# Kernel tuning notes

Measured on AMD Instinct MI355X. Metric: run time of the kernel, lower is better.

Reference implementation:

```python
import jax, jax.numpy as jnp
import numpy as np
import math

M = 0.5
S = 64.0
COS_M = math.cos(M)
SIN_M = math.sin(M)
THRESHOLD = math.cos(math.pi - M)
MM = math.sin(math.pi - M) * M

B, D, N_CLASSES = 512, 512, 100000


def setup_inputs() -> dict:
    key = jax.random.key(0)
    k1, k2, k3 = jax.random.split(key, 3)
    embeddings = jax.random.normal(k1, (B, D), dtype=jnp.float32)
    labels = jax.random.randint(k2, (B,), 0, N_CLASSES, dtype=jnp.int32)
    kernel = jax.random.normal(k3, (D, N_CLASSES), dtype=jnp.float32) * 0.05
    t = jnp.zeros((), dtype=jnp.float32)
    return {"embeddings": embeddings, "labels": labels, "kernel": kernel, "t": t}


def reference(embeddings, labels, kernel, t):
    # L2 normalize embeddings (rows) and kernel (columns)
    emb = embeddings / jnp.linalg.norm(embeddings, axis=1, keepdims=True)
    kn = kernel / jnp.linalg.norm(kernel, axis=0, keepdims=True)
    cos_theta = jnp.clip(emb @ kn, -1.0, 1.0)  # [B, C]

    b = cos_theta.shape[0]
    rows = jnp.arange(b)
    target_logit = cos_theta[rows, labels][:, None]  # [B, 1]
    sin_theta = jnp.sqrt(1.0 - jnp.square(target_logit))
    cos_theta_m = target_logit * COS_M - sin_theta * SIN_M  # [B, 1]

    mask = cos_theta > cos_theta_m  # [B, C] hard examples
    final_target_logit = jnp.where(target_logit > THRESHOLD,
                                   cos_theta_m, target_logit - MM)  # [B, 1]

    # EMA update of t (assigned before the hard-example scaling in TF code)
    new_t = 0.01 * jnp.mean(target_logit) + 0.99 * t

    # hard examples: c -> c * (t + c); others unchanged
    cos_theta = jnp.where(mask, cos_theta * (new_t + cos_theta), cos_theta)
    # overwrite label column with the margin-adjusted target logit
    cos_theta = cos_theta.at[rows, labels].set(final_target_logit[:, 0])
    return cos_theta * S
```

## Files before the change

kernel.cpp:

```cpp
#include <hip/hip_runtime.h>
#include <hip/hip_bf16.h>
#include <cstdint>
#include <cstddef>

#define C_N 100000
#define B_N 512
#define D_N 512

#define COS_M_F   0.87758256189037276f
#define SIN_M_F   0.47942553860420301f
#define THRESH_F  (-0.87758256189037276f)
#define MM_F      0.23971276930210150f
#define S_F       64.0f

typedef __attribute__((ext_vector_type(8))) short short8;
typedef __attribute__((ext_vector_type(4))) float f32x4;

__device__ __forceinline__ unsigned short f2bf(float f) {
  unsigned u = __float_as_uint(f);
  u = u + 0x7fffu + ((u >> 16) & 1u);
  return (unsigned short)(u >> 16);
}

__device__ __forceinline__ float wave_sum(float v) {
#pragma unroll
  for (int o = 32; o > 0; o >>= 1) v += __shfl_down(v, o, 64);
  return v;
}

__device__ __forceinline__ void lds_load16(const void* g, void* l) {
  __builtin_amdgcn_global_load_lds(
      (const __attribute__((address_space(1))) unsigned int*)g,
      (__attribute__((address_space(3))) unsigned int*)l, 16, 0, 0);
}

__global__ void embnorm_k(const float* __restrict__ emb, unsigned short* __restrict__ embn,
                          float* __restrict__ rinv) {
  int row = blockIdx.x;
  int t = threadIdx.x;
  float4 v = ((const float4*)(emb + (size_t)row * D_N))[t];
  float ss = v.x * v.x + v.y * v.y + v.z * v.z + v.w * v.w;
  ss = wave_sum(ss);
  __shared__ float red[2];
  if ((t & 63) == 0) red[t >> 6] = ss;
  __syncthreads();
  float tot = red[0] + red[1];
  float ri = rsqrtf(tot);
  if (t == 0) rinv[row] = ri;
  ushort4 o;
  o.x = f2bf(v.x * ri); o.y = f2bf(v.y * ri); o.z = f2bf(v.z * ri); o.w = f2bf(v.w * ri);
  ((ushort4*)(embn + (size_t)row * D_N))[t] = o;
}

__global__ void target2_k(const float* __restrict__ emb, const float* __restrict__ Kp,
                          const float* __restrict__ rinv, const int* __restrict__ labels,
                          float* __restrict__ target, float* __restrict__ ctm,
                          float* __restrict__ ft) {
  int row = blockIdx.x;
  int t = threadIdx.x;
  int lab = labels[row];
  float p = 0.f, ss = 0.f;
  for (int d = t; d < D_N; d += 256) {
    float kv = Kp[(size_t)d * C_N + lab];
    p = fmaf(emb[(size_t)row * D_N + d], kv, p);
    ss = fmaf(kv, kv, ss);
  }
  p = wave_sum(p);
  ss = wave_sum(ss);
  __shared__ float redp[4], reds[4];
  if ((t & 63) == 0) { redp[t >> 6] = p; reds[t >> 6] = ss; }
  __syncthreads();
  if (t == 0) {
    float dot = redp[0] + redp[1] + redp[2] + redp[3];
    float sums = reds[0] + reds[1] + reds[2] + reds[3];
    float tg = dot * rinv[row] * rsqrtf(fmaxf(sums, 1e-30f));
    tg = fminf(fmaxf(tg, -1.f), 1.f);
    float st = sqrtf(fmaxf(1.f - tg * tg, 0.f));
    float cm = tg * COS_M_F - st * SIN_M_F;
    float f = (tg > THRESH_F) ? cm : (tg - MM_F);
    target[row] = tg;
    ctm[row] = cm;
    ft[row] = f;
  }
}

__global__ void newt_k(const float* __restrict__ target, const float* __restrict__ t_in,
                       float* __restrict__ newt) {
  int t = threadIdx.x;
  float v = target[t];
  v = wave_sum(v);
  __shared__ float red[8];
  if ((t & 63) == 0) red[t >> 6] = v;
  __syncthreads();
  if (t == 0) {
    float s = 0.f;
#pragma unroll
    for (int i = 0; i < 8; ++i) s += red[i];
    *newt = 0.01f * (s / (float)B_N) + 0.99f * t_in[0];
  }
}

__launch_bounds__(512, 2)
__global__ void gemm3_k(const float* __restrict__ Kp,
                        const unsigned short* __restrict__ embn,
                        const int* __restrict__ labels,
                        const float* __restrict__ ctm, const float* __restrict__ ft,
                        const float* __restrict__ newt_p, float* __restrict__ out) {
  __shared__ __align__(16) char lds[131072 + 3 * 2048 + 256];
  unsigned short* Bl = (unsigned short*)lds;
  unsigned short* Albase = (unsigned short*)(lds + 65536);
  float* ssum = (float*)(lds + 65536);
  int*   slab = (int*)(lds + 131072);
  float* sctm = (float*)(lds + 131072 + 2048);
  float* sft  = (float*)(lds + 131072 + 4096);
  float* cns  = (float*)(lds + 131072 + 6144);

  const int t = threadIdx.x;
  const int j0 = blockIdx.x * 64;

  slab[t] = labels[t];
  sctm[t] = ctm[t];
  sft[t]  = ft[t];

  const int jq = t & 15;
  const int dr = t >> 4;
  const int jcol = min((j0 >> 2) + jq, (C_N >> 2) - 1);
  const float4* __restrict__ Kv = (const float4*)Kp;
  float4 v[16];
#pragma unroll
  for (int i = 0; i < 16; ++i)
    v[i] = Kv[(size_t)(dr * 16 + i) * (C_N / 4) + jcol];

  float s0 = 0.f, s1 = 0.f, s2 = 0.f, s3 = 0.f;
#pragma unroll
  for (int i = 0; i < 16; ++i) {
    s0 = fmaf(v[i].x, v[i].x, s0);
    s1 = fmaf(v[i].y, v[i].y, s1);
    s2 = fmaf(v[i].z, v[i].z, s2);
    s3 = fmaf(v[i].w, v[i].w, s3);
  }
  ssum[dr * 64 + jq * 4 + 0] = s0;
  ssum[dr * 64 + jq * 4 + 1] = s1;
  ssum[dr * 64 + jq * 4 + 2] = s2;
  ssum[dr * 64 + jq * 4 + 3] = s3;
  __syncthreads();
  if (t < 64) {
    float s = 0.f;
#pragma unroll
    for (int d = 0; d < 32; ++d) s += ssum[d * 64 + t];
    cns[t] = rsqrtf(fmaxf(s, 1e-30f));
  }
  __syncthreads();

  const int l = t & 63, w = t >> 6;
  const int sidx = (l & 7) ^ (l >> 3);
  const int r0 = ((l >> 3) << 1) | (sidx >> 2);
  const int kc8 = (sidx & 3) * 8;
  const unsigned short* asrc = embn + (size_t)(w * 64 + r0) * D_N + kc8;

#pragma unroll
  for (int p = 0; p < 4; ++p)
    lds_load16(asrc + p * 16 * D_N, Albase + w * 2048 + p * 512);

  {
    const float rc0 = cns[jq * 4 + 0];
    const float rc1 = cns[jq * 4 + 1];
    const float rc2 = cns[jq * 4 + 2];
    const float rc3 = cns[jq * 4 + 3];
    const int itile = dr >> 1;
    const int cbase = (dr & 1) * 2;
#pragma unroll
    for (int cc = 0; cc < 4; ++cc) {
      const int n = jq * 4 + cc;
      const int rowp = n >> 1;
      const int nb = (n & 1) << 2;
      const int x7 = rowp & 7;
      const float rc = (cc == 0) ? rc0 : (cc == 1) ? rc1 : (cc == 2) ? rc2 : rc3;
#pragma unroll
      for (int h = 0; h < 2; ++h) {
        unsigned w0 = (unsigned)f2bf(v[h * 8 + 0][cc] * rc) | ((unsigned)f2bf(v[h * 8 + 1][cc] * rc) << 16);
        unsigned w1 = (unsigned)f2bf(v[h * 8 + 2][cc] * rc) | ((unsigned)f2bf(v[h * 8 + 3][cc] * rc) << 16);
        unsigned w2 = (unsigned)f2bf(v[h * 8 + 4][cc] * rc) | ((unsigned)f2bf(v[h * 8 + 5][cc] * rc) << 16);
        unsigned w3 = (unsigned)f2bf(v[h * 8 + 6][cc] * rc) | ((unsigned)f2bf(v[h * 8 + 7][cc] * rc) << 16);
        char* dst = (char*)Bl + itile * 4096 + rowp * 128 + ((nb | (cbase + h)) ^ x7) * 16;
        *(uint4*)dst = make_uint4(w0, w1, w2, w3);
      }
    }
  }
  __syncthreads();

  const int wr = w >> 1, wc = w & 1;
  const int lq = l >> 4, lr = l & 15;
  const int s16 = ((((lr & 1) << 2) | lq) ^ (lr >> 1)) << 4;
  const int rh = lr >> 1;
  const float newt = *newt_p;

  f32x4 acc[8][2];
#pragma unroll
  for (int mb = 0; mb < 8; ++mb) {
    acc[mb][0] = 0;
    acc[mb][1] = 0;
  }

#pragma unroll
  for (int it = 0; it < 16; ++it) {
    const int cur = it & 1, nxt = cur ^ 1;
    if (it < 15) {
      const int k0 = (it + 1) * 32;
#pragma unroll
      for (int p = 0; p < 4; ++p)
        lds_load16(asrc + p * 16 * D_N + k0, Albase + nxt * 16384 + w * 2048 + p * 512);
    }
    const char* Ab = (const char*)(Albase + cur * 16384);
    const char* Bt = (const char*)Bl + it * 4096;
    short8 b0 = *(const short8*)(Bt + ((wc * 16 + 0 + rh) << 7) + s16);
    short8 b1 = *(const short8*)(Bt + ((wc * 16 + 8 + rh) << 7) + s16);
#pragma unroll
    for (int mb = 0; mb < 8; ++mb) {
      short8 a = *(const short8*)(Ab + ((wr * 64 + mb * 8 + rh) << 7) + s16);
      acc[mb][0] = __builtin_amdgcn_mfma_f32_16x16x32_bf16(a, b0, acc[mb][0], 0, 0, 0);
      acc[mb][1] = __builtin_amdgcn_mfma_f32_16x16x32_bf16(a, b1, acc[mb][1], 0, 0, 0);
    }
    __syncthreads();
  }

  const int jn0 = j0 + wc * 32 + lr;
  const int jn1 = jn0 + 16;
#pragma unroll
  for (int mb = 0; mb < 8; ++mb) {
    int ibase = wr * 128 + mb * 16 + 4 * lq;
#pragma unroll
    for (int r = 0; r < 4; ++r) {
      int i = ibase + r;
      int lab = slab[i];
      float cm = sctm[i];
      float f = sft[i];
      {
        float c = fminf(fmaxf(acc[mb][0][r], -1.f), 1.f);
        float o = (c > cm) ? c * (newt + c) : c;
        o = (jn0 == lab) ? f : o;
        if (jn0 < C_N)
          __builtin_nontemporal_store(o * S_F, &out[(size_t)i * C_N + jn0]);
      }
      {
        float c = fminf(fmaxf(acc[mb][1][r], -1.f), 1.f);
        float o = (c > cm) ? c * (newt + c) : c;
        o = (jn1 == lab) ? f : o;
        if (jn1 < C_N)
          __builtin_nontemporal_store(o * S_F, &out[(size_t)i * C_N + jn1]);
      }
    }
  }
}

extern "C" void kernel_launch(void* const* d_in, const int* in_sizes, int n_in,
                              void* d_out, int out_size, void* d_ws, size_t ws_size,
                              hipStream_t stream) {
  (void)in_sizes; (void)n_in; (void)out_size; (void)ws_size;
  const float* emb = (const float*)d_in[0];
  const int* labels = (const int*)d_in[1];
  const float* Kp = (const float*)d_in[2];
  const float* t_in = (const float*)d_in[3];
  float* out = (float*)d_out;

  char* wsp = (char*)d_ws;
  unsigned short* embn = (unsigned short*)(wsp + 0);
  float* target = (float*)(wsp + 524288);
  float* ctm    = (float*)(wsp + 526336);
  float* ft     = (float*)(wsp + 528384);
  float* rinv   = (float*)(wsp + 530432);
  float* newt   = (float*)(wsp + 532480);

  embnorm_k<<<B_N, 128, 0, stream>>>(emb, embn, rinv);
  target2_k<<<B_N, 256, 0, stream>>>(emb, Kp, rinv, labels, target, ctm, ft);
  newt_k<<<1, 512, 0, stream>>>(target, t_in, newt);
  gemm3_k<<<(C_N + 63) / 64, 512, 0, stream>>>(Kp, embn, labels, ctm, ft, newt, out);
}
```

Before: 176.8 us.

## Read normalized embeddings directly from global memory instead of staging in LDS

Removes the double-buffered LDS staging of the bf16 embedding tile (global_load_lds plus per-iteration barriers). A-fragments are now loaded straight from global memory, relying on L2 since every block reads the same 512 KB matrix. This halves LDS use and raises the launch bound to 4 blocks per CU to gain occupancy. Nontemporal output stores become plain stores. The risk is higher global/L2 load latency inside the MFMA loop and cache pollution from the large output write.

```diff
diff --git a/kernel.cpp b/kernel.cpp
--- a/kernel.cpp
+++ b/kernel.cpp
@@ -26,12 +26,6 @@
 #pragma unroll
   for (int o = 32; o > 0; o >>= 1) v += __shfl_down(v, o, 64);
   return v;
-}
-
-__device__ __forceinline__ void lds_load16(const void* g, void* l) {
-  __builtin_amdgcn_global_load_lds(
-      (const __attribute__((address_space(1))) unsigned int*)g,
-      (__attribute__((address_space(3))) unsigned int*)l, 16, 0, 0);
 }
 
 __global__ void embnorm_k(const float* __restrict__ emb, unsigned short* __restrict__ embn,
@@ -100,20 +94,19 @@
   }
 }
 
-__launch_bounds__(512, 2)
-__global__ void gemm3_k(const float* __restrict__ Kp,
+__launch_bounds__(512, 4)
+__global__ void gemm4_k(const float* __restrict__ Kp,
                         const unsigned short* __restrict__ embn,
                         const int* __restrict__ labels,
                         const float* __restrict__ ctm, const float* __restrict__ ft,
                         const float* __restrict__ newt_p, float* __restrict__ out) {
-  __shared__ __align__(16) char lds[131072 + 3 * 2048 + 256];
+  __shared__ __align__(16) char lds[65536 + 3 * 2048 + 256];
   unsigned short* Bl = (unsigned short*)lds;
-  unsigned short* Albase = (unsigned short*)(lds + 65536);
-  float* ssum = (float*)(lds + 65536);
-  int*   slab = (int*)(lds + 131072);
-  float* sctm = (float*)(lds + 131072 + 2048);
-  float* sft  = (float*)(lds + 131072 + 4096);
-  float* cns  = (float*)(lds + 131072 + 6144);
+  float* ssum = (float*)lds;
+  int*   slab = (int*)(lds + 65536);
+  float* sctm = (float*)(lds + 65536 + 2048);
+  float* sft  = (float*)(lds + 65536 + 4096);
+  float* cns  = (float*)(lds + 65536 + 6144);
 
   const int t = threadIdx.x;
   const int j0 = blockIdx.x * 64;
@@ -151,16 +144,6 @@
     cns[t] = rsqrtf(fmaxf(s, 1e-30f));
   }
   __syncthreads();
-
-  const int l = t & 63, w = t >> 6;
-  const int sidx = (l & 7) ^ (l >> 3);
-  const int r0 = ((l >> 3) << 1) | (sidx >> 2);
-  const int kc8 = (sidx & 3) * 8;
-  const unsigned short* asrc = embn + (size_t)(w * 64 + r0) * D_N + kc8;
-
-#pragma unroll
-  for (int p = 0; p < 4; ++p)
-    lds_load16(asrc + p * 16 * D_N, Albase + w * 2048 + p * 512);
 
   {
     const float rc0 = cns[jq * 4 + 0];
@@ -189,12 +172,15 @@
   }
   __syncthreads();
 
+  const int l = t & 63, w = t >> 6;
   const int wr = w >> 1, wc = w & 1;
   const int lq = l >> 4, lr = l & 15;
   const int s16 = ((((lr & 1) << 2) | lq) ^ (lr >> 1)) << 4;
   const int rh = lr >> 1;
   const float newt = *newt_p;
 
+  const unsigned short* abase = embn + (size_t)(wr * 128 + lr) * D_N + lq * 8;
+
   f32x4 acc[8][2];
 #pragma unroll
   for (int mb = 0; mb < 8; ++mb) {
@@ -204,24 +190,15 @@
 
 #pragma unroll
   for (int it = 0; it < 16; ++it) {
-    const int cur = it & 1, nxt = cur ^ 1;
-    if (it < 15) {
-      const int k0 = (it + 1) * 32;
-#pragma unroll
-      for (int p = 0; p < 4; ++p)
-        lds_load16(asrc + p * 16 * D_N + k0, Albase + nxt * 16384 + w * 2048 + p * 512);
-    }
-    const char* Ab = (const char*)(Albase + cur * 16384);
     const char* Bt = (const char*)Bl + it * 4096;
     short8 b0 = *(const short8*)(Bt + ((wc * 16 + 0 + rh) << 7) + s16);
     short8 b1 = *(const short8*)(Bt + ((wc * 16 + 8 + rh) << 7) + s16);
 #pragma unroll
     for (int mb = 0; mb < 8; ++mb) {
-      short8 a = *(const short8*)(Ab + ((wr * 64 + mb * 8 + rh) << 7) + s16);
+      short8 a = *(const short8*)(abase + (size_t)mb * 16 * D_N + it * 32);
       acc[mb][0] = __builtin_amdgcn_mfma_f32_16x16x32_bf16(a, b0, acc[mb][0], 0, 0, 0);
       acc[mb][1] = __builtin_amdgcn_mfma_f32_16x16x32_bf16(a, b1, acc[mb][1], 0, 0, 0);
     }
-    __syncthreads();
   }
 
   const int jn0 = j0 + wc * 32 + lr;
@@ -239,15 +216,13 @@
         float c = fminf(fmaxf(acc[mb][0][r], -1.f), 1.f);
         float o = (c > cm) ? c * (newt + c) : c;
         o = (jn0 == lab) ? f : o;
-        if (jn0 < C_N)
-          __builtin_nontemporal_store(o * S_F, &out[(size_t)i * C_N + jn0]);
+        if (jn0 < C_N) out[(size_t)i * C_N + jn0] = o * S_F;
       }
       {
         float c = fminf(fmaxf(acc[mb][1][r], -1.f), 1.f);
         float o = (c > cm) ? c * (newt + c) : c;
         o = (jn1 == lab) ? f : o;
-        if (jn1 < C_N)
-          __builtin_nontemporal_store(o * S_F, &out[(size_t)i * C_N + jn1]);
+        if (jn1 < C_N) out[(size_t)i * C_N + jn1] = o * S_F;
       }
     }
   }
@@ -274,5 +249,5 @@
   embnorm_k<<<B_N, 128, 0, stream>>>(emb, embn, rinv);
   target2_k<<<B_N, 256, 0, stream>>>(emb, Kp, rinv, labels, target, ctm, ft);
   newt_k<<<1, 512, 0, stream>>>(target, t_in, newt);
-  gemm3_k<<<(C_N + 63) / 64, 512, 0, stream>>>(Kp, embn, labels, ctm, ft, newt, out);
-}
+  gemm4_k<<<(C_N + 63) / 64, 512, 0, stream>>>(Kp, embn, labels, ctm, ft, newt, out);
+}
```

Result: slower. 294.7 us (+66.7%).

## Pre-normalize kernel into transposed bf16 buffer and widen GEMM tile with coalesced stores

Applied to the files above, without the earlier changes.

Splits the kernel-column normalization into a separate pass that writes a transposed bf16 copy of the weight matrix to workspace. The GEMM then streams both operands through LDS with async loads, uses 1024-thread blocks covering 128 columns, and stages results in LDS so each output row is written with coalesced 16-byte stores. The aim is better output store efficiency and a simpler GEMM main loop. The cost is an extra pass that writes and re-reads about 100 MB of bf16 weights.

```diff
diff --git a/kernel.cpp b/kernel.cpp
--- a/kernel.cpp
+++ b/kernel.cpp
@@ -32,6 +32,82 @@
   __builtin_amdgcn_global_load_lds(
       (const __attribute__((address_space(1))) unsigned int*)g,
       (__attribute__((address_space(3))) unsigned int*)l, 16, 0, 0);
+}
+
+__launch_bounds__(512)
+__global__ void knorm2_k(const float* __restrict__ Kp, float* __restrict__ cninv,
+                         unsigned short* __restrict__ Knt) {
+  __shared__ __align__(16) unsigned short Tl[64 * 512];
+  __shared__ float ssum[32][64];
+  __shared__ float cns[64];
+
+  const int t = threadIdx.x;
+  const int j0 = blockIdx.x * 64;
+  const int jq = t & 15;
+  const int dr = t >> 4;
+  const int jcol = min((j0 >> 2) + jq, (C_N >> 2) - 1);
+  const float4* __restrict__ Kv = (const float4*)Kp;
+
+  float4 v[16];
+#pragma unroll
+  for (int i = 0; i < 16; ++i)
+    v[i] = Kv[(size_t)(dr * 16 + i) * (C_N / 4) + jcol];
+
+  float s0 = 0.f, s1 = 0.f, s2 = 0.f, s3 = 0.f;
+#pragma unroll
+  for (int i = 0; i < 16; ++i) {
+    s0 = fmaf(v[i].x, v[i].x, s0);
+    s1 = fmaf(v[i].y, v[i].y, s1);
+    s2 = fmaf(v[i].z, v[i].z, s2);
+    s3 = fmaf(v[i].w, v[i].w, s3);
+  }
+  ssum[dr][jq * 4 + 0] = s0;
+  ssum[dr][jq * 4 + 1] = s1;
+  ssum[dr][jq * 4 + 2] = s2;
+  ssum[dr][jq * 4 + 3] = s3;
+  __syncthreads();
+  if (t < 64) {
+    float s = 0.f;
+#pragma unroll
+    for (int d = 0; d < 32; ++d) s += ssum[d][t];
+    float r = rsqrtf(fmaxf(s, 1e-30f));
+    cns[t] = r;
+    if (j0 + t < C_N) cninv[j0 + t] = r;
+  }
+  __syncthreads();
+
+  const float r0 = cns[jq * 4 + 0];
+  const float r1 = cns[jq * 4 + 1];
+  const float r2 = cns[jq * 4 + 2];
+  const float r3 = cns[jq * 4 + 3];
+#pragma unroll
+  for (int g = 0; g < 4; ++g) {
+    const int ch = dr * 2 + (g >> 1);
+    const int sub = (g & 1) * 8;
+#pragma unroll
+    for (int c = 0; c < 4; ++c) {
+      const int j = jq * 4 + c;
+      const float rc = (c == 0) ? r0 : (c == 1) ? r1 : (c == 2) ? r2 : r3;
+      unsigned lo, hi;
+      lo = (unsigned)f2bf(v[g * 4 + 0][c] * rc) | ((unsigned)f2bf(v[g * 4 + 1][c] * rc) << 16);
+      hi = (unsigned)f2bf(v[g * 4 + 2][c] * rc) | ((unsigned)f2bf(v[g * 4 + 3][c] * rc) << 16);
+      const int phys = ch ^ (j & 7);
+      *(uint2*)((char*)Tl + j * 1024 + phys * 16 + sub) = make_uint2(lo, hi);
+    }
+  }
+  __syncthreads();
+
+  const int jr = t >> 3;
+  const int dc = t & 7;
+  const int jg = j0 + jr;
+  if (jg < C_N) {
+#pragma unroll
+    for (int s = 0; s < 8; ++s) {
+      const int phys = (s * 8) + (dc ^ (jr & 7));
+      uint4 val = *(const uint4*)((const char*)Tl + jr * 1024 + phys * 16);
+      *(uint4*)(&Knt[(size_t)jg * D_N + s * 64 + dc * 8]) = val;
+    }
+  }
 }
 
 __global__ void embnorm_k(const float* __restrict__ emb, unsigned short* __restrict__ embn,
@@ -100,100 +176,37 @@
   }
 }
 
-__launch_bounds__(512, 2)
-__global__ void gemm3_k(const float* __restrict__ Kp,
+__launch_bounds__(1024, 4)
+__global__ void gemm8_k(const unsigned short* __restrict__ Knt,
                         const unsigned short* __restrict__ embn,
                         const int* __restrict__ labels,
                         const float* __restrict__ ctm, const float* __restrict__ ft,
                         const float* __restrict__ newt_p, float* __restrict__ out) {
-  __shared__ __align__(16) char lds[131072 + 3 * 2048 + 256];
-  unsigned short* Bl = (unsigned short*)lds;
-  unsigned short* Albase = (unsigned short*)(lds + 65536);
-  float* ssum = (float*)(lds + 65536);
-  int*   slab = (int*)(lds + 131072);
-  float* sctm = (float*)(lds + 131072 + 2048);
-  float* sft  = (float*)(lds + 131072 + 4096);
-  float* cns  = (float*)(lds + 131072 + 6144);
+  __shared__ __align__(16) char lds[81920];
+  unsigned short* Al = (unsigned short*)lds;
+  unsigned short* Bb = (unsigned short*)(lds + 65536);
 
   const int t = threadIdx.x;
-  const int j0 = blockIdx.x * 64;
-
-  slab[t] = labels[t];
-  sctm[t] = ctm[t];
-  sft[t]  = ft[t];
-
-  const int jq = t & 15;
-  const int dr = t >> 4;
-  const int jcol = min((j0 >> 2) + jq, (C_N >> 2) - 1);
-  const float4* __restrict__ Kv = (const float4*)Kp;
-  float4 v[16];
-#pragma unroll
-  for (int i = 0; i < 16; ++i)
-    v[i] = Kv[(size_t)(dr * 16 + i) * (C_N / 4) + jcol];
-
-  float s0 = 0.f, s1 = 0.f, s2 = 0.f, s3 = 0.f;
-#pragma unroll
-  for (int i = 0; i < 16; ++i) {
-    s0 = fmaf(v[i].x, v[i].x, s0);
-    s1 = fmaf(v[i].y, v[i].y, s1);
-    s2 = fmaf(v[i].z, v[i].z, s2);
-    s3 = fmaf(v[i].w, v[i].w, s3);
-  }
-  ssum[dr * 64 + jq * 4 + 0] = s0;
-  ssum[dr * 64 + jq * 4 + 1] = s1;
-  ssum[dr * 64 + jq * 4 + 2] = s2;
-  ssum[dr * 64 + jq * 4 + 3] = s3;
-  __syncthreads();
-  if (t < 64) {
-    float s = 0.f;
-#pragma unroll
-    for (int d = 0; d < 32; ++d) s += ssum[d * 64 + t];
-    cns[t] = rsqrtf(fmaxf(s, 1e-30f));
-  }
-  __syncthreads();
-
   const int l = t & 63, w = t >> 6;
+  const int j0 = blockIdx.x * 128;
+
   const int sidx = (l & 7) ^ (l >> 3);
   const int r0 = ((l >> 3) << 1) | (sidx >> 2);
   const int kc8 = (sidx & 3) * 8;
-  const unsigned short* asrc = embn + (size_t)(w * 64 + r0) * D_N + kc8;
-
-#pragma unroll
-  for (int p = 0; p < 4; ++p)
-    lds_load16(asrc + p * 16 * D_N, Albase + w * 2048 + p * 512);
-
-  {
-    const float rc0 = cns[jq * 4 + 0];
-    const float rc1 = cns[jq * 4 + 1];
-    const float rc2 = cns[jq * 4 + 2];
-    const float rc3 = cns[jq * 4 + 3];
-    const int itile = dr >> 1;
-    const int cbase = (dr & 1) * 2;
-#pragma unroll
-    for (int cc = 0; cc < 4; ++cc) {
-      const int n = jq * 4 + cc;
-      const int rowp = n >> 1;
-      const int nb = (n & 1) << 2;
-      const int x7 = rowp & 7;
-      const float rc = (cc == 0) ? rc0 : (cc == 1) ? rc1 : (cc == 2) ? rc2 : rc3;
-#pragma unroll
-      for (int h = 0; h < 2; ++h) {
-        unsigned w0 = (unsigned)f2bf(v[h * 8 + 0][cc] * rc) | ((unsigned)f2bf(v[h * 8 + 1][cc] * rc) << 16);
-        unsigned w1 = (unsigned)f2bf(v[h * 8 + 2][cc] * rc) | ((unsigned)f2bf(v[h * 8 + 3][cc] * rc) << 16);
-        unsigned w2 = (unsigned)f2bf(v[h * 8 + 4][cc] * rc) | ((unsigned)f2bf(v[h * 8 + 5][cc] * rc) << 16);
-        unsigned w3 = (unsigned)f2bf(v[h * 8 + 6][cc] * rc) | ((unsigned)f2bf(v[h * 8 + 7][cc] * rc) << 16);
-        char* dst = (char*)Bl + itile * 4096 + rowp * 128 + ((nb | (cbase + h)) ^ x7) * 16;
-        *(uint4*)dst = make_uint4(w0, w1, w2, w3);
-      }
-    }
-  }
-  __syncthreads();
-
-  const int wr = w >> 1, wc = w & 1;
+
+  const unsigned short* asrc = embn + (size_t)(w * 32 + r0) * D_N + kc8;
+  const unsigned short* bsrc = Knt + (size_t)(j0 + (w & 7) * 16 + r0) * D_N + kc8;
+
+#pragma unroll
+  for (int p = 0; p < 2; ++p)
+    lds_load16(asrc + p * 16 * D_N, Al + w * 1024 + p * 512);
+  if (w < 8) lds_load16(bsrc, Bb + w * 512);
+  __syncthreads();
+
+  const int wr = w >> 2, wc = w & 3;
   const int lq = l >> 4, lr = l & 15;
   const int s16 = ((((lr & 1) << 2) | lq) ^ (lr >> 1)) << 4;
   const int rh = lr >> 1;
-  const float newt = *newt_p;
 
   f32x4 acc[8][2];
 #pragma unroll
@@ -208,11 +221,12 @@
     if (it < 15) {
       const int k0 = (it + 1) * 32;
 #pragma unroll
-      for (int p = 0; p < 4; ++p)
-        lds_load16(asrc + p * 16 * D_N + k0, Albase + nxt * 16384 + w * 2048 + p * 512);
-    }
-    const char* Ab = (const char*)(Albase + cur * 16384);
-    const char* Bt = (const char*)Bl + it * 4096;
+      for (int p = 0; p < 2; ++p)
+        lds_load16(asrc + p * 16 * D_N + k0, Al + nxt * 16384 + w * 1024 + p * 512);
+      if (w < 8) lds_load16(bsrc + k0, Bb + nxt * 4096 + w * 512);
+    }
+    const char* Ab = (const char*)(Al + cur * 16384);
+    const char* Bt = (const char*)(Bb + cur * 4096);
     short8 b0 = *(const short8*)(Bt + ((wc * 16 + 0 + rh) << 7) + s16);
     short8 b1 = *(const short8*)(Bt + ((wc * 16 + 8 + rh) << 7) + s16);
 #pragma unroll
@@ -224,32 +238,51 @@
     __syncthreads();
   }
 
-  const int jn0 = j0 + wc * 32 + lr;
-  const int jn1 = jn0 + 16;
-#pragma unroll
-  for (int mb = 0; mb < 8; ++mb) {
-    int ibase = wr * 128 + mb * 16 + 4 * lq;
-#pragma unroll
-    for (int r = 0; r < 4; ++r) {
-      int i = ibase + r;
-      int lab = slab[i];
-      float cm = sctm[i];
-      float f = sft[i];
-      {
-        float c = fminf(fmaxf(acc[mb][0][r], -1.f), 1.f);
-        float o = (c > cm) ? c * (newt + c) : c;
-        o = (jn0 == lab) ? f : o;
-        if (jn0 < C_N)
-          __builtin_nontemporal_store(o * S_F, &out[(size_t)i * C_N + jn0]);
+  const float newt = *newt_p;
+  float* Tl = (float*)lds;
+  const int row_l = t >> 3;
+  const int sgl = t & 7;
+  const int rx = row_l & 7;
+
+#pragma unroll
+  for (int pp = 0; pp < 4; ++pp) {
+    if (wr == pp) {
+#pragma unroll
+      for (int mb = 0; mb < 8; ++mb) {
+#pragma unroll
+        for (int nb = 0; nb < 2; ++nb) {
+          const int seg = nb * 4 + (lr >> 2);
+          const int e = lr & 3;
+#pragma unroll
+          for (int r = 0; r < 4; ++r) {
+            const int rl = mb * 16 + lq * 4 + r;
+            const int ps = seg ^ (rl & 7);
+            Tl[rl * 128 + wc * 32 + ps * 4 + e] = acc[mb][nb][r];
+          }
+        }
       }
-      {
-        float c = fminf(fmaxf(acc[mb][1][r], -1.f), 1.f);
-        float o = (c > cm) ? c * (newt + c) : c;
-        o = (jn1 == lab) ? f : o;
-        if (jn1 < C_N)
-          __builtin_nontemporal_store(o * S_F, &out[(size_t)i * C_N + jn1]);
+    }
+    __syncthreads();
+    const int grow = pp * 128 + row_l;
+    const int lab = labels[grow];
+    const float cm = ctm[grow];
+    const float f = ft[grow];
+#pragma unroll
+    for (int k = 0; k < 4; ++k) {
+      const int jb = j0 + k * 32 + sgl * 4;
+      if (jb < C_N) {
+        f32x4 vv = *(const f32x4*)&Tl[row_l * 128 + k * 32 + (sgl ^ rx) * 4];
+#pragma unroll
+        for (int e = 0; e < 4; ++e) {
+          float c = fminf(fmaxf(vv[e], -1.f), 1.f);
+          float o = (c > cm) ? c * (newt + c) : c;
+          o = (jb + e == lab) ? f : o;
+          vv[e] = o * S_F;
+        }
+        *(f32x4*)&out[(size_t)grow * C_N + jb] = vv;
       }
     }
+    __syncthreads();
   }
 }
 
@@ -264,15 +297,19 @@
   float* out = (float*)d_out;
 
   char* wsp = (char*)d_ws;
-  unsigned short* embn = (unsigned short*)(wsp + 0);
-  float* target = (float*)(wsp + 524288);
-  float* ctm    = (float*)(wsp + 526336);
-  float* ft     = (float*)(wsp + 528384);
-  float* rinv   = (float*)(wsp + 530432);
-  float* newt   = (float*)(wsp + 532480);
-
+  const size_t KNT_BYTES = (size_t)100096 * D_N * 2;
+  unsigned short* Knt = (unsigned short*)(wsp + 0);
+  unsigned short* embn = (unsigned short*)(wsp + KNT_BYTES);
+  float* cninv  = (float*)(wsp + KNT_BYTES + 524288);
+  float* target = (float*)(wsp + KNT_BYTES + 524288 + 400000);
+  float* ctm    = (float*)(wsp + KNT_BYTES + 524288 + 400000 + 2048);
+  float* ft     = (float*)(wsp + KNT_BYTES + 524288 + 400000 + 2 * 2048);
+  float* rinv   = (float*)(wsp + KNT_BYTES + 524288 + 400000 + 3 * 2048);
+  float* newt   = (float*)(wsp + KNT_BYTES + 524288 + 400000 + 4 * 2048);
+
+  knorm2_k<<<(C_N + 63) / 64, 512, 0, stream>>>(Kp, cninv, Knt);
   embnorm_k<<<B_N, 128, 0, stream>>>(emb, embn, rinv);
   target2_k<<<B_N, 256, 0, stream>>>(emb, Kp, rinv, labels, target, ctm, ft);
   newt_k<<<1, 512, 0, stream>>>(target, t_in, newt);
-  gemm3_k<<<(C_N + 63) / 64, 512, 0, stream>>>(Kp, embn, labels, ctm, ft, newt, out);
-}
+  gemm8_k<<<(C_N + 127) / 128, 1024, 0, stream>>>(Knt, embn, labels, ctm, ft, newt, out);
+}
```

Result: slower. 201.2 us (+13.8%).
